# Performance work log

Measured on AMD Instinct MI355X. Metric: run time of the kernel, lower is better.

The kernel has to match this reference:

```python
import jax, jax.numpy as jnp
import numpy as np

UNITS = 100000
S = 64.0
M1 = 1.0
M2 = 0.5
M3 = 0.0


def setup_inputs() -> dict:
    key = jax.random.key(0)
    k1, k2, k3 = jax.random.split(key, 3)
    inputs = jax.random.normal(k1, (512, 512), dtype=jnp.float32)
    label = jax.random.randint(k2, (512,), 0, UNITS, dtype=jnp.int64)
    # fc7 weight, init stddev 0.01 as in the original layer
    w = jax.random.normal(k3, (512, UNITS), dtype=jnp.float32) * 0.01
    return {"inputs": inputs, "label": label, "w": w}


def reference(inputs, label, w):
    # L2-normalize embeddings (rows) and weights (columns)
    emb = inputs / jnp.linalg.norm(inputs, axis=-1, keepdims=True)
    wn = w / jnp.linalg.norm(w, axis=0, keepdims=True)
    # fc7 = s * cos(theta), shape [batch, units]
    fc7 = jnp.matmul(emb * S, wn)
    # ArcFace margin branch (m1=1.0, m2=0.5, m3=0.0)
    cos_t = fc7 / S
    t = jnp.arccos(cos_t)
    if M1 != 1.0:
        t = t * M1
    if M2 > 0.0:
        t = t + M2
    body = jnp.cos(t)
    if M3 > 0.0:
        body = body - M3
    diff = body * S - fc7
    one_hot = jax.nn.one_hot(label, UNITS, dtype=fc7.dtype)
    fc7 = fc7 + one_hot * diff
    return jax.nn.softmax(fc7, axis=-1)
```

## Files before the change

### kernel.cpp

```cpp
#include <hip/hip_runtime.h>
#include <math.h>

#define UNITS 100000
#define BATCH 512
#define DIM 512
#define BN 64
#define NBLK ((UNITS + BN - 1) / BN)
#define SCALE 64.0f
#define COS_M2 0.87758256189037271612f
#define SIN_M2 0.47942553860420300027f
#define LOG2E  1.44269504088896340736f

typedef _Float16 half8 __attribute__((ext_vector_type(8)));
typedef float floatx4 __attribute__((ext_vector_type(4)));

__global__ void norm_emb_k(const float* __restrict__ inp, _Float16* __restrict__ A2) {
    const int row = blockIdx.x;
    const int lane = threadIdx.x;
    const float* rp = inp + row * DIM + lane * 8;
    float v[8];
#pragma unroll
    for (int j = 0; j < 8; ++j) v[j] = rp[j];
    float ss = 0.f;
#pragma unroll
    for (int j = 0; j < 8; ++j) ss += v[j] * v[j];
#pragma unroll
    for (int off = 32; off > 0; off >>= 1) ss += __shfl_xor(ss, off);
    const float inv = 1.0f / sqrtf(ss);
    half8 h;
#pragma unroll
    for (int j = 0; j < 8; ++j) h[j] = (_Float16)(v[j] * inv);
    const int idx = ((((row >> 4) * 16 + (lane >> 2)) * 64) + (row & 15) + 16 * (lane & 3)) * 8;
    *(half8*)(A2 + idx) = h;
}

template<bool HALF>
__global__ __launch_bounds__(512, 4) void gemm_exp_k(
    const float* __restrict__ w, const _Float16* __restrict__ A2,
    const int* __restrict__ label,
    float* __restrict__ outf, _Float16* __restrict__ outh,
    float* __restrict__ psum, float* __restrict__ pmax) {
    __shared__ _Float16 Bt[64][64][8];
    __shared__ float scratch[32][68];
    __shared__ float cninv_s[64];

    const int t = threadIdx.x;
    const int blk = blockIdx.x;
    const int c0 = blk * BN;
    const int kk = t >> 4;
    const int ci = t & 15;

    bool valid[4];
#pragma unroll
    for (int j = 0; j < 4; ++j) valid[j] = (c0 + ci + 16 * j) < UNITS;

    float sq[4] = {0.f, 0.f, 0.f, 0.f};
    float va[4][4], vb[4][4];

    auto issue = [&](int g, float (*dst)[4]) {
#pragma unroll
        for (int c = 0; c < 4; ++c) {
            const float* p = w + (size_t)((g * 4 + c) * 32 + kk) * UNITS + c0 + ci;
#pragma unroll
            for (int j = 0; j < 4; ++j) dst[c][j] = valid[j] ? p[16 * j] : 0.f;
        }
    };
    auto consume = [&](int g, float (*src)[4]) {
#pragma unroll
        for (int c = 0; c < 4; ++c) {
            const int k = (g * 4 + c) * 32 + kk;
#pragma unroll
            for (int j = 0; j < 4; ++j) {
                const float x = src[c][j];
                sq[j] += x * x;
                Bt[k >> 3][ci + 16 * j][k & 7] = (_Float16)x;
            }
        }
    };
    issue(0, va);
    issue(1, vb);
    consume(0, va);
    issue(2, va);
    consume(1, vb);
    issue(3, vb);
    consume(2, va);
    consume(3, vb);

#pragma unroll
    for (int j = 0; j < 4; ++j) scratch[kk][ci + 16 * j] = sq[j];
    __syncthreads();
    if (t < 64) {
        float s = 0.f;
#pragma unroll
        for (int k2 = 0; k2 < 32; ++k2) s += scratch[k2][t];
        cninv_s[t] = 1.0f / sqrtf(s);
    }
    __syncthreads();

    const int wid = t >> 6;
    const int lane = t & 63;
    const int colg = lane & 15;
    const int rowg = lane >> 4;
    const int rowbase = wid * 64;

    floatx4 acc[4][4];
#pragma unroll
    for (int mf = 0; mf < 4; ++mf)
#pragma unroll
        for (int nf = 0; nf < 4; ++nf) acc[mf][nf] = (floatx4){0.f, 0.f, 0.f, 0.f};

#pragma unroll 2
    for (int ks = 0; ks < 16; ++ks) {
        half8 b[4];
#pragma unroll
        for (int nf = 0; nf < 4; ++nf)
            b[nf] = *(const half8*)(&Bt[ks * 4 + rowg][nf * 16 + colg][0]);
#pragma unroll
        for (int mf = 0; mf < 4; ++mf) {
            const half8 a = *(const half8*)(A2 + ((((wid * 4 + mf) * 16) + ks) * 64 + lane) * 8);
#pragma unroll
            for (int nf = 0; nf < 4; ++nf)
                acc[mf][nf] = __builtin_amdgcn_mfma_f32_16x16x32_f16(a, b[nf], acc[mf][nf], 0, 0, 0);
        }
    }

    float inv_cn[4];
#pragma unroll
    for (int nf = 0; nf < 4; ++nf) inv_cn[nf] = cninv_s[nf * 16 + colg];

#pragma unroll
    for (int mf = 0; mf < 4; ++mf) {
#pragma unroll
        for (int r = 0; r < 4; ++r) {
            const int R = rowbase + mf * 16 + rowg * 4 + r;
            const int labv = label[R];
            float lg[4];
            float mx = -1e30f;
#pragma unroll
            for (int nf = 0; nf < 4; ++nf) {
                const int C = c0 + nf * 16 + colg;
                float cs = acc[mf][nf][r] * inv_cn[nf];
                float x;
                if (C == labv) {
                    cs = fminf(1.f, fmaxf(-1.f, cs));
                    x = SCALE * (cs * COS_M2 - sqrtf(fmaxf(0.f, 1.f - cs * cs)) * SIN_M2);
                } else {
                    x = SCALE * cs;
                }
                if (C >= UNITS) x = -1e30f;
                lg[nf] = x;
                mx = fmaxf(mx, x);
            }
            mx = fmaxf(mx, __shfl_xor(mx, 1));
            mx = fmaxf(mx, __shfl_xor(mx, 2));
            mx = fmaxf(mx, __shfl_xor(mx, 4));
            mx = fmaxf(mx, __shfl_xor(mx, 8));
            float s = 0.f;
#pragma unroll
            for (int nf = 0; nf < 4; ++nf) {
                const int C = c0 + nf * 16 + colg;
                const float e = exp2f((lg[nf] - mx) * LOG2E);
                s += (C < UNITS) ? e : 0.f;
                if (C < UNITS) {
                    if (HALF) outh[(size_t)R * UNITS + C] = (_Float16)e;
                    else      outf[(size_t)R * UNITS + C] = e;
                }
            }
            s += __shfl_xor(s, 1);
            s += __shfl_xor(s, 2);
            s += __shfl_xor(s, 4);
            s += __shfl_xor(s, 8);
            if (colg == 0) {
                psum[R * NBLK + blk] = s;
                pmax[R * NBLK + blk] = mx;
            }
        }
    }
}

__global__ void rowfac_k(const float* __restrict__ psum, const float* __restrict__ pmax,
                         float* __restrict__ fac) {
    const int row = blockIdx.x;
    const int lane = threadIdx.x;
    float mx = -1e30f;
    for (int b = lane; b < NBLK; b += 64) mx = fmaxf(mx, pmax[row * NBLK + b]);
#pragma unroll
    for (int off = 32; off > 0; off >>= 1) mx = fmaxf(mx, __shfl_xor(mx, off));
    float s = 0.f;
    for (int b = lane; b < NBLK; b += 64)
        s += psum[row * NBLK + b] * exp2f((pmax[row * NBLK + b] - mx) * LOG2E);
#pragma unroll
    for (int off = 32; off > 0; off >>= 1) s += __shfl_xor(s, off);
    const float invS = 1.0f / s;
    for (int b = lane; b < NBLK; b += 64)
        fac[row * NBLK + b] = exp2f((pmax[row * NBLK + b] - mx) * LOG2E) * invS;
}

__global__ void scale_half_k(const _Float16* __restrict__ v, const float* __restrict__ fac,
                             float* __restrict__ out) {
    const int row = blockIdx.y;
    const int c = (blockIdx.x * 256 + threadIdx.x) * 8;
    if (c >= UNITS) return;
    const float f = fac[row * NBLK + (c >> 6)];
    const half8 h = *(const half8*)(v + (size_t)row * UNITS + c);
    float4 o1, o2;
    o1.x = (float)h[0] * f; o1.y = (float)h[1] * f; o1.z = (float)h[2] * f; o1.w = (float)h[3] * f;
    o2.x = (float)h[4] * f; o2.y = (float)h[5] * f; o2.z = (float)h[6] * f; o2.w = (float)h[7] * f;
    float* op = out + (size_t)row * UNITS + c;
    *(float4*)op = o1;
    *(float4*)(op + 4) = o2;
}

__global__ void scale_f32_k(float* __restrict__ out, const float* __restrict__ fac) {
    const int row = blockIdx.y;
    const int c = (blockIdx.x * 256 + threadIdx.x) * 8;
    if (c >= UNITS) return;
    const float f = fac[row * NBLK + (c >> 6)];
    float* op = out + (size_t)row * UNITS + c;
    float4 o1 = *(float4*)op;
    float4 o2 = *(float4*)(op + 4);
    o1.x *= f; o1.y *= f; o1.z *= f; o1.w *= f;
    o2.x *= f; o2.y *= f; o2.z *= f; o2.w *= f;
    *(float4*)op = o1;
    *(float4*)(op + 4) = o2;
}

extern "C" void kernel_launch(void* const* d_in, const int* in_sizes, int n_in,
                              void* d_out, int out_size, void* d_ws, size_t ws_size,
                              hipStream_t stream) {
    const float* inp   = (const float*)d_in[0];
    const int*   label = (const int*)d_in[1];
    const float* w     = (const float*)d_in[2];
    float* out = (float*)d_out;

    char* ws = (char*)d_ws;
    _Float16* A2   = (_Float16*)ws;
    float* psum    = (float*)(ws + (1 << 20));
    float* pmax    = (float*)(ws + (1 << 20) + 4 * BATCH * NBLK);
    float* fac     = (float*)(ws + (1 << 20) + 8 * BATCH * NBLK);
    _Float16* vh   = (_Float16*)(ws + (16 << 20));
    const size_t need = (size_t)(16 << 20) + (size_t)BATCH * UNITS * 2;
    const bool half_path = ws_size >= need;

    norm_emb_k<<<BATCH, 64, 0, stream>>>(inp, A2);
    if (half_path)
        gemm_exp_k<true><<<NBLK, 512, 0, stream>>>(w, A2, label, out, vh, psum, pmax);
    else
        gemm_exp_k<false><<<NBLK, 512, 0, stream>>>(w, A2, label, out, vh, psum, pmax);
    rowfac_k<<<BATCH, 64, 0, stream>>>(psum, pmax, fac);
    dim3 sg((UNITS + 2047) / 2048, BATCH);
    if (half_path)
        scale_half_k<<<sg, 256, 0, stream>>>(vh, fac, out);
    else
        scale_f32_k<<<sg, 256, 0, stream>>>(out, fac);
}
```

Before: 233.6 us.

## Pre-convert weights to fp16 tiles and stage GEMM outputs through LDS

Adds a separate wprep kernel that reads the fp32 weight matrix once. It computes the column inverse norms and writes an fp16 copy in the MFMA-ready tile layout. The GEMM kernel then loads each 64 KB tile straight into LDS with global_load_lds. Exponentials are written to a per-wave LDS bounce buffer first, so global stores become 16-byte vectors instead of scattered 2-byte writes, and the logit scale is folded into the embedding normalization. In exchange there is an extra kernel and an extra fp16 write and read of the whole weight matrix through HBM.

```diff
diff --git a/kernel.cpp b/kernel.cpp
--- a/kernel.cpp
+++ b/kernel.cpp
@@ -26,7 +26,7 @@
     for (int j = 0; j < 8; ++j) ss += v[j] * v[j];
 #pragma unroll
     for (int off = 32; off > 0; off >>= 1) ss += __shfl_xor(ss, off);
-    const float inv = 1.0f / sqrtf(ss);
+    const float inv = SCALE / sqrtf(ss);
     half8 h;
 #pragma unroll
     for (int j = 0; j < 8; ++j) h[j] = (_Float16)(v[j] * inv);
@@ -34,118 +34,129 @@
     *(half8*)(A2 + idx) = h;
 }
 
-template<bool HALF>
-__global__ __launch_bounds__(512, 4) void gemm_exp_k(
-    const float* __restrict__ w, const _Float16* __restrict__ A2,
-    const int* __restrict__ label,
-    float* __restrict__ outf, _Float16* __restrict__ outh,
-    float* __restrict__ psum, float* __restrict__ pmax) {
-    __shared__ _Float16 Bt[64][64][8];
-    __shared__ float scratch[32][68];
-    __shared__ float cninv_s[64];
-
+__global__ __launch_bounds__(256) void wprep_k(const float* __restrict__ w,
+                                               _Float16* __restrict__ w16,
+                                               float* __restrict__ cninv) {
+    __shared__ float T[128 * 66];
     const int t = threadIdx.x;
     const int blk = blockIdx.x;
     const int c0 = blk * BN;
-    const int kk = t >> 4;
-    const int ci = t & 15;
-
-    bool valid[4];
-#pragma unroll
-    for (int j = 0; j < 4; ++j) valid[j] = (c0 + ci + 16 * j) < UNITS;
-
-    float sq[4] = {0.f, 0.f, 0.f, 0.f};
-    float va[4][4], vb[4][4];
-
-    auto issue = [&](int g, float (*dst)[4]) {
-#pragma unroll
-        for (int c = 0; c < 4; ++c) {
-            const float* p = w + (size_t)((g * 4 + c) * 32 + kk) * UNITS + c0 + ci;
-#pragma unroll
-            for (int j = 0; j < 4; ++j) dst[c][j] = valid[j] ? p[16 * j] : 0.f;
-        }
-    };
-    auto consume = [&](int g, float (*src)[4]) {
-#pragma unroll
-        for (int c = 0; c < 4; ++c) {
-            const int k = (g * 4 + c) * 32 + kk;
-#pragma unroll
-            for (int j = 0; j < 4; ++j) {
-                const float x = src[c][j];
-                sq[j] += x * x;
-                Bt[k >> 3][ci + 16 * j][k & 7] = (_Float16)x;
-            }
-        }
-    };
-    issue(0, va);
-    issue(1, vb);
-    consume(0, va);
-    issue(2, va);
-    consume(1, vb);
-    issue(3, vb);
-    consume(2, va);
-    consume(3, vb);
-
-#pragma unroll
-    for (int j = 0; j < 4; ++j) scratch[kk][ci + 16 * j] = sq[j];
+    const int cl = (t & 31) * 2;
+    const int kr = t >> 5;
+    const bool cval = (c0 + cl + 1) < UNITS;
+    float sq0 = 0.f, sq1 = 0.f;
+
+    for (int q = 0; q < 4; ++q) {
+#pragma unroll
+        for (int ps = 0; ps < 16; ++ps) {
+            const int k = q * 128 + ps * 8 + kr;
+            float2 rd = cval ? *(const float2*)(w + (size_t)k * UNITS + c0 + cl)
+                             : make_float2(0.f, 0.f);
+            sq0 += rd.x * rd.x;
+            sq1 += rd.y * rd.y;
+            *(float2*)&T[(ps * 8 + kr) * 66 + cl] = rd;
+        }
+        __syncthreads();
+#pragma unroll
+        for (int g = 0; g < 4; ++g) {
+            const int G = t + 256 * g;
+            const int col = G & 63;
+            const int rowg = (G >> 6) & 3;
+            const int ksl = G >> 8;
+            half8 h;
+#pragma unroll
+            for (int e = 0; e < 8; ++e)
+                h[e] = (_Float16)T[(ksl * 32 + rowg * 8 + e) * 66 + col];
+            const int off = blk * 32768 + (((q * 4 + ksl) * 4 + rowg) * 64 + col) * 8;
+            *(half8*)(w16 + off) = h;
+        }
+        __syncthreads();
+    }
+    T[(t >> 5) * 66 + cl] = sq0;
+    T[(t >> 5) * 66 + cl + 1] = sq1;
     __syncthreads();
     if (t < 64) {
         float s = 0.f;
 #pragma unroll
-        for (int k2 = 0; k2 < 32; ++k2) s += scratch[k2][t];
-        cninv_s[t] = 1.0f / sqrtf(s);
-    }
-    __syncthreads();
-
+        for (int gi = 0; gi < 8; ++gi) s += T[gi * 66 + t];
+        cninv[c0 + t] = (s > 0.f) ? rsqrtf(s) : 1.0f;
+    }
+}
+
+template<bool HALF>
+__global__ __launch_bounds__(512, 4) void gemm2_k(
+    const _Float16* __restrict__ w16, const _Float16* __restrict__ A2,
+    const int* __restrict__ label, const float* __restrict__ cninv,
+    float* __restrict__ outf, _Float16* __restrict__ vh,
+    float* __restrict__ psum, float* __restrict__ pmax) {
+    __shared__ char smem[73728];
+    _Float16* Bt = (_Float16*)smem;
+
+    const int t = threadIdx.x;
+    const int blk = blockIdx.x;
+    const int c0 = blk * BN;
     const int wid = t >> 6;
     const int lane = t & 63;
     const int colg = lane & 15;
     const int rowg = lane >> 4;
     const int rowbase = wid * 64;
 
+    const char* gsrc = (const char*)w16 + (size_t)blk * 65536;
+#pragma unroll
+    for (int j = 0; j < 8; ++j) {
+        const int chunk = wid * 8 + j;
+        __builtin_amdgcn_global_load_lds(
+            (const __attribute__((address_space(1))) void*)(gsrc + chunk * 1024 + lane * 16),
+            (__attribute__((address_space(3))) void*)(smem + chunk * 1024 + lane * 16),
+            16, 0, 0);
+    }
+
+    float cn[4];
+#pragma unroll
+    for (int nf = 0; nf < 4; ++nf) cn[nf] = cninv[c0 + nf * 16 + colg];
+
+    asm volatile("s_waitcnt vmcnt(0)" ::: "memory");
+    __syncthreads();
+
     floatx4 acc[4][4];
 #pragma unroll
     for (int mf = 0; mf < 4; ++mf)
 #pragma unroll
         for (int nf = 0; nf < 4; ++nf) acc[mf][nf] = (floatx4){0.f, 0.f, 0.f, 0.f};
 
-#pragma unroll 2
+#pragma unroll 4
     for (int ks = 0; ks < 16; ++ks) {
         half8 b[4];
 #pragma unroll
         for (int nf = 0; nf < 4; ++nf)
-            b[nf] = *(const half8*)(&Bt[ks * 4 + rowg][nf * 16 + colg][0]);
+            b[nf] = *(const half8*)(Bt + ((ks * 4 + rowg) * 64 + nf * 16 + colg) * 8);
 #pragma unroll
         for (int mf = 0; mf < 4; ++mf) {
-            const half8 a = *(const half8*)(A2 + ((((wid * 4 + mf) * 16) + ks) * 64 + lane) * 8);
+            const half8 a = *(const half8*)(A2 + (((wid * 4 + mf) * 16 + ks) * 64 + lane) * 8);
 #pragma unroll
             for (int nf = 0; nf < 4; ++nf)
                 acc[mf][nf] = __builtin_amdgcn_mfma_f32_16x16x32_f16(a, b[nf], acc[mf][nf], 0, 0, 0);
         }
     }
-
-    float inv_cn[4];
-#pragma unroll
-    for (int nf = 0; nf < 4; ++nf) inv_cn[nf] = cninv_s[nf * 16 + colg];
-
+    __syncthreads();
+
+    _Float16* bounce = (_Float16*)smem + wid * 4608;
 #pragma unroll
     for (int mf = 0; mf < 4; ++mf) {
 #pragma unroll
         for (int r = 0; r < 4; ++r) {
-            const int R = rowbase + mf * 16 + rowg * 4 + r;
+            const int lrow = mf * 16 + rowg * 4 + r;
+            const int R = rowbase + lrow;
             const int labv = label[R];
             float lg[4];
             float mx = -1e30f;
 #pragma unroll
             for (int nf = 0; nf < 4; ++nf) {
                 const int C = c0 + nf * 16 + colg;
-                float cs = acc[mf][nf][r] * inv_cn[nf];
-                float x;
+                float x = acc[mf][nf][r] * cn[nf];
                 if (C == labv) {
-                    cs = fminf(1.f, fmaxf(-1.f, cs));
+                    float cs = fminf(1.f, fmaxf(-1.f, x * (1.0f / SCALE)));
                     x = SCALE * (cs * COS_M2 - sqrtf(fmaxf(0.f, 1.f - cs * cs)) * SIN_M2);
-                } else {
-                    x = SCALE * cs;
                 }
                 if (C >= UNITS) x = -1e30f;
                 lg[nf] = x;
@@ -161,10 +172,7 @@
                 const int C = c0 + nf * 16 + colg;
                 const float e = exp2f((lg[nf] - mx) * LOG2E);
                 s += (C < UNITS) ? e : 0.f;
-                if (C < UNITS) {
-                    if (HALF) outh[(size_t)R * UNITS + C] = (_Float16)e;
-                    else      outf[(size_t)R * UNITS + C] = e;
-                }
+                bounce[lrow * 72 + nf * 16 + colg] = (_Float16)e;
             }
             s += __shfl_xor(s, 1);
             s += __shfl_xor(s, 2);
@@ -173,6 +181,29 @@
             if (colg == 0) {
                 psum[R * NBLK + blk] = s;
                 pmax[R * NBLK + blk] = mx;
+            }
+        }
+    }
+    __syncthreads();
+
+    const int rl = lane >> 3;
+    const int ch = lane & 7;
+#pragma unroll
+    for (int p = 0; p < 8; ++p) {
+        const int row_l = p * 8 + rl;
+        const int Rg = rowbase + row_l;
+        const int C8 = c0 + ch * 8;
+        const half8 h = *(const half8*)((_Float16*)smem + wid * 4608 + row_l * 72 + ch * 8);
+        if (C8 + 7 < UNITS) {
+            if (HALF) {
+                *(half8*)(vh + (size_t)Rg * UNITS + C8) = h;
+            } else {
+                float4 o1, o2;
+                o1.x = (float)h[0]; o1.y = (float)h[1]; o1.z = (float)h[2]; o1.w = (float)h[3];
+                o2.x = (float)h[4]; o2.y = (float)h[5]; o2.z = (float)h[6]; o2.w = (float)h[7];
+                float* op = outf + (size_t)Rg * UNITS + C8;
+                *(float4*)op = o1;
+                *(float4*)(op + 4) = o2;
             }
         }
     }
@@ -236,17 +267,20 @@
     char* ws = (char*)d_ws;
     _Float16* A2   = (_Float16*)ws;
     float* psum    = (float*)(ws + (1 << 20));
-    float* pmax    = (float*)(ws + (1 << 20) + 4 * BATCH * NBLK);
-    float* fac     = (float*)(ws + (1 << 20) + 8 * BATCH * NBLK);
-    _Float16* vh   = (_Float16*)(ws + (16 << 20));
-    const size_t need = (size_t)(16 << 20) + (size_t)BATCH * UNITS * 2;
+    float* pmax    = (float*)(ws + (1 << 20) + 4u * BATCH * NBLK);
+    float* fac     = (float*)(ws + (1 << 20) + 8u * BATCH * NBLK);
+    float* cninv   = (float*)(ws + (1 << 20) + 12u * BATCH * NBLK);
+    _Float16* w16  = (_Float16*)(ws + (16 << 20));
+    _Float16* vh   = (_Float16*)(ws + (size_t)(16 << 20) + (size_t)NBLK * 65536);
+    const size_t need = (size_t)(16 << 20) + (size_t)NBLK * 65536 + (size_t)BATCH * UNITS * 2;
     const bool half_path = ws_size >= need;
 
     norm_emb_k<<<BATCH, 64, 0, stream>>>(inp, A2);
+    wprep_k<<<NBLK, 256, 0, stream>>>(w, w16, cninv);
     if (half_path)
-        gemm_exp_k<true><<<NBLK, 512, 0, stream>>>(w, A2, label, out, vh, psum, pmax);
+        gemm2_k<true><<<NBLK, 512, 0, stream>>>(w16, A2, label, cninv, out, vh, psum, pmax);
     else
-        gemm_exp_k<false><<<NBLK, 512, 0, stream>>>(w, A2, label, out, vh, psum, pmax);
+        gemm2_k<false><<<NBLK, 512, 0, stream>>>(w16, A2, label, cninv, out, vh, psum, pmax);
     rowfac_k<<<BATCH, 64, 0, stream>>>(psum, pmax, fac);
     dim3 sg((UNITS + 2047) / 2048, BATCH);
     if (half_path)
```

Result: slower. 325.9 us (+39.5%).

## Pipeline weight loads with MFMA via double-buffered LDS and coalesce half stores

Applied to the files above, without the earlier changes.

The GEMM kernel now streams the weight columns in eight K-chunks through a double-buffered LDS tile, so global loads for later chunks overlap with MFMA work on the current chunk. Before, all loads and conversions finished before any matrix math started. The fp16 exp values are staged through LDS and written out as 16-byte row segments instead of scattered 2-byte stores. The per-block partial sums and maxima are written transposed and contiguous, and the scale factor is folded into embedding normalisation. The cost is more barriers and extra LDS traffic, plus a 16-byte store path that assumes the unit count is a multiple of 8.

```diff
diff --git a/kernel.cpp b/kernel.cpp
--- a/kernel.cpp
+++ b/kernel.cpp
@@ -14,6 +14,11 @@
 typedef _Float16 half8 __attribute__((ext_vector_type(8)));
 typedef float floatx4 __attribute__((ext_vector_type(4)));
 
+#define PHASE_BARRIER() do { \
+    asm volatile("s_waitcnt lgkmcnt(0)" ::: "memory"); \
+    __builtin_amdgcn_s_barrier(); \
+} while (0)
+
 __global__ void norm_emb_k(const float* __restrict__ inp, _Float16* __restrict__ A2) {
     const int row = blockIdx.x;
     const int lane = threadIdx.x;
@@ -26,7 +31,7 @@
     for (int j = 0; j < 8; ++j) ss += v[j] * v[j];
 #pragma unroll
     for (int off = 32; off > 0; off >>= 1) ss += __shfl_xor(ss, off);
-    const float inv = 1.0f / sqrtf(ss);
+    const float inv = SCALE / sqrtf(ss);
     half8 h;
 #pragma unroll
     for (int j = 0; j < 8; ++j) h[j] = (_Float16)(v[j] * inv);
@@ -35,117 +40,114 @@
 }
 
 template<bool HALF>
-__global__ __launch_bounds__(512, 4) void gemm_exp_k(
+__global__ __launch_bounds__(512, 4) void gemmfused_k(
     const float* __restrict__ w, const _Float16* __restrict__ A2,
     const int* __restrict__ label,
-    float* __restrict__ outf, _Float16* __restrict__ outh,
+    _Float16* __restrict__ vh, float* __restrict__ outf,
     float* __restrict__ psum, float* __restrict__ pmax) {
-    __shared__ _Float16 Bt[64][64][8];
-    __shared__ float scratch[32][68];
+    __shared__ _Float16 Bt[2][512 * 8];
+    __shared__ float sqred[8][64];
     __shared__ float cninv_s[64];
+    __shared__ float sums_s[512];
+    __shared__ float maxs_s[512];
 
     const int t = threadIdx.x;
     const int blk = blockIdx.x;
     const int c0 = blk * BN;
-    const int kk = t >> 4;
-    const int ci = t & 15;
-
-    bool valid[4];
-#pragma unroll
-    for (int j = 0; j < 4; ++j) valid[j] = (c0 + ci + 16 * j) < UNITS;
-
-    float sq[4] = {0.f, 0.f, 0.f, 0.f};
-    float va[4][4], vb[4][4];
-
-    auto issue = [&](int g, float (*dst)[4]) {
-#pragma unroll
-        for (int c = 0; c < 4; ++c) {
-            const float* p = w + (size_t)((g * 4 + c) * 32 + kk) * UNITS + c0 + ci;
-#pragma unroll
-            for (int j = 0; j < 4; ++j) dst[c][j] = valid[j] ? p[16 * j] : 0.f;
-        }
+    const int w8 = t >> 6;
+    const int lane = t & 63;
+    const int colg = lane & 15;
+    const int rowg = lane >> 4;
+
+    const bool cval = (c0 + lane) < UNITS;
+    const float* wbase = w + (cval ? (c0 + lane) : (UNITS - 1));
+
+    float sq = 0.f;
+    float rs[2][8];
+
+    auto LOADC = [&](int ch, float* r) {
+#pragma unroll
+        for (int i = 0; i < 8; ++i)
+            r[i] = wbase[(size_t)(ch * 64 + w8 * 8 + i) * UNITS];
     };
-    auto consume = [&](int g, float (*src)[4]) {
-#pragma unroll
-        for (int c = 0; c < 4; ++c) {
-            const int k = (g * 4 + c) * 32 + kk;
-#pragma unroll
-            for (int j = 0; j < 4; ++j) {
-                const float x = src[c][j];
-                sq[j] += x * x;
-                Bt[k >> 3][ci + 16 * j][k & 7] = (_Float16)x;
-            }
-        }
+    auto WRITEC = [&](const float* r, int buf) {
+        half8 h;
+#pragma unroll
+        for (int i = 0; i < 8; ++i) {
+            const float x = cval ? r[i] : 0.f;
+            sq += x * x;
+            h[i] = (_Float16)x;
+        }
+        *(half8*)&Bt[buf][(w8 * 64 + lane) * 8] = h;
     };
-    issue(0, va);
-    issue(1, vb);
-    consume(0, va);
-    issue(2, va);
-    consume(1, vb);
-    issue(3, vb);
-    consume(2, va);
-    consume(3, vb);
-
-#pragma unroll
-    for (int j = 0; j < 4; ++j) scratch[kk][ci + 16 * j] = sq[j];
+
+    floatx4 acc[4][4];
+#pragma unroll
+    for (int mf = 0; mf < 4; ++mf)
+#pragma unroll
+        for (int nf = 0; nf < 4; ++nf) acc[mf][nf] = (floatx4){0.f, 0.f, 0.f, 0.f};
+
+    auto MFMAC = [&](int ch, int buf) {
+#pragma unroll
+        for (int ksl = 0; ksl < 2; ++ksl) {
+            half8 b[4];
+#pragma unroll
+            for (int nf = 0; nf < 4; ++nf)
+                b[nf] = *(const half8*)&Bt[buf][((ksl * 4 + rowg) * 64 + nf * 16 + colg) * 8];
+#pragma unroll
+            for (int mf = 0; mf < 4; ++mf) {
+                const half8 a = *(const half8*)(A2 +
+                    (size_t)(((w8 * 4 + mf) * 16 + ch * 2 + ksl) * 64 + lane) * 8);
+#pragma unroll
+                for (int nf = 0; nf < 4; ++nf)
+                    acc[mf][nf] = __builtin_amdgcn_mfma_f32_16x16x32_f16(a, b[nf], acc[mf][nf], 0, 0, 0);
+            }
+        }
+    };
+
+    LOADC(0, rs[0]);
+    LOADC(1, rs[1]);
+    WRITEC(rs[0], 0);
+    PHASE_BARRIER();
+#pragma unroll
+    for (int ch = 0; ch < 8; ++ch) {
+        if (ch + 2 < 8) LOADC(ch + 2, rs[ch & 1]);
+        if (ch + 1 < 8) WRITEC(rs[1 - (ch & 1)], (ch + 1) & 1);
+        MFMAC(ch, ch & 1);
+        PHASE_BARRIER();
+    }
+
+    sqred[w8][lane] = sq;
     __syncthreads();
     if (t < 64) {
         float s = 0.f;
 #pragma unroll
-        for (int k2 = 0; k2 < 32; ++k2) s += scratch[k2][t];
-        cninv_s[t] = 1.0f / sqrtf(s);
+        for (int g = 0; g < 8; ++g) s += sqred[g][t];
+        cninv_s[t] = rsqrtf(s);
     }
     __syncthreads();
 
-    const int wid = t >> 6;
-    const int lane = t & 63;
-    const int colg = lane & 15;
-    const int rowg = lane >> 4;
-    const int rowbase = wid * 64;
-
-    floatx4 acc[4][4];
-#pragma unroll
-    for (int mf = 0; mf < 4; ++mf)
-#pragma unroll
-        for (int nf = 0; nf < 4; ++nf) acc[mf][nf] = (floatx4){0.f, 0.f, 0.f, 0.f};
-
-#pragma unroll 2
-    for (int ks = 0; ks < 16; ++ks) {
-        half8 b[4];
-#pragma unroll
-        for (int nf = 0; nf < 4; ++nf)
-            b[nf] = *(const half8*)(&Bt[ks * 4 + rowg][nf * 16 + colg][0]);
-#pragma unroll
-        for (int mf = 0; mf < 4; ++mf) {
-            const half8 a = *(const half8*)(A2 + ((((wid * 4 + mf) * 16) + ks) * 64 + lane) * 8);
-#pragma unroll
-            for (int nf = 0; nf < 4; ++nf)
-                acc[mf][nf] = __builtin_amdgcn_mfma_f32_16x16x32_f16(a, b[nf], acc[mf][nf], 0, 0, 0);
-        }
-    }
-
-    float inv_cn[4];
-#pragma unroll
-    for (int nf = 0; nf < 4; ++nf) inv_cn[nf] = cninv_s[nf * 16 + colg];
+    float cn[4];
+#pragma unroll
+    for (int nf = 0; nf < 4; ++nf) cn[nf] = cninv_s[nf * 16 + colg];
+
+    _Float16* bounce = &Bt[0][0] + w8 * 1024;
 
 #pragma unroll
     for (int mf = 0; mf < 4; ++mf) {
 #pragma unroll
         for (int r = 0; r < 4; ++r) {
-            const int R = rowbase + mf * 16 + rowg * 4 + r;
+            const int R = w8 * 64 + mf * 16 + rowg * 4 + r;
             const int labv = label[R];
             float lg[4];
             float mx = -1e30f;
 #pragma unroll
             for (int nf = 0; nf < 4; ++nf) {
                 const int C = c0 + nf * 16 + colg;
-                float cs = acc[mf][nf][r] * inv_cn[nf];
-                float x;
+                float x = acc[mf][nf][r] * cn[nf];
                 if (C == labv) {
-                    cs = fminf(1.f, fmaxf(-1.f, cs));
+                    float cs = fminf(1.f, fmaxf(-1.f, x * (1.0f / SCALE)));
                     x = SCALE * (cs * COS_M2 - sqrtf(fmaxf(0.f, 1.f - cs * cs)) * SIN_M2);
-                } else {
-                    x = SCALE * cs;
                 }
                 if (C >= UNITS) x = -1e30f;
                 lg[nf] = x;
@@ -161,21 +163,31 @@
                 const int C = c0 + nf * 16 + colg;
                 const float e = exp2f((lg[nf] - mx) * LOG2E);
                 s += (C < UNITS) ? e : 0.f;
-                if (C < UNITS) {
-                    if (HALF) outh[(size_t)R * UNITS + C] = (_Float16)e;
-                    else      outf[(size_t)R * UNITS + C] = e;
-                }
+                if (HALF) bounce[(rowg * 4 + r) * 64 + nf * 16 + colg] = (_Float16)e;
+                else if (C < UNITS) outf[(size_t)R * UNITS + C] = e;
             }
             s += __shfl_xor(s, 1);
             s += __shfl_xor(s, 2);
             s += __shfl_xor(s, 4);
             s += __shfl_xor(s, 8);
-            if (colg == 0) {
-                psum[R * NBLK + blk] = s;
-                pmax[R * NBLK + blk] = mx;
+            if (colg == 0) { sums_s[R] = s; maxs_s[R] = mx; }
+        }
+        if (HALF) {
+#pragma unroll
+            for (int p = 0; p < 2; ++p) {
+                const int row_l = p * 8 + (lane >> 3);
+                const int seg = lane & 7;
+                const half8 hv = *(const half8*)&bounce[row_l * 64 + seg * 8];
+                const int gc = c0 + seg * 8;
+                if (gc + 8 <= UNITS)
+                    *(half8*)(vh + (size_t)(w8 * 64 + mf * 16 + row_l) * UNITS + gc) = hv;
             }
         }
     }
+
+    __syncthreads();
+    psum[(size_t)blk * BATCH + t] = sums_s[t];
+    pmax[(size_t)blk * BATCH + t] = maxs_s[t];
 }
 
 __global__ void rowfac_k(const float* __restrict__ psum, const float* __restrict__ pmax,
@@ -183,17 +195,17 @@
     const int row = blockIdx.x;
     const int lane = threadIdx.x;
     float mx = -1e30f;
-    for (int b = lane; b < NBLK; b += 64) mx = fmaxf(mx, pmax[row * NBLK + b]);
+    for (int b = lane; b < NBLK; b += 64) mx = fmaxf(mx, pmax[(size_t)b * BATCH + row]);
 #pragma unroll
     for (int off = 32; off > 0; off >>= 1) mx = fmaxf(mx, __shfl_xor(mx, off));
     float s = 0.f;
     for (int b = lane; b < NBLK; b += 64)
-        s += psum[row * NBLK + b] * exp2f((pmax[row * NBLK + b] - mx) * LOG2E);
+        s += psum[(size_t)b * BATCH + row] * exp2f((pmax[(size_t)b * BATCH + row] - mx) * LOG2E);
 #pragma unroll
     for (int off = 32; off > 0; off >>= 1) s += __shfl_xor(s, off);
     const float invS = 1.0f / s;
     for (int b = lane; b < NBLK; b += 64)
-        fac[row * NBLK + b] = exp2f((pmax[row * NBLK + b] - mx) * LOG2E) * invS;
+        fac[(size_t)row * NBLK + b] = exp2f((pmax[(size_t)b * BATCH + row] - mx) * LOG2E) * invS;
 }
 
 __global__ void scale_half_k(const _Float16* __restrict__ v, const float* __restrict__ fac,
@@ -201,7 +213,7 @@
     const int row = blockIdx.y;
     const int c = (blockIdx.x * 256 + threadIdx.x) * 8;
     if (c >= UNITS) return;
-    const float f = fac[row * NBLK + (c >> 6)];
+    const float f = fac[(size_t)row * NBLK + (c >> 6)];
     const half8 h = *(const half8*)(v + (size_t)row * UNITS + c);
     float4 o1, o2;
     o1.x = (float)h[0] * f; o1.y = (float)h[1] * f; o1.z = (float)h[2] * f; o1.w = (float)h[3] * f;
@@ -215,7 +227,7 @@
     const int row = blockIdx.y;
     const int c = (blockIdx.x * 256 + threadIdx.x) * 8;
     if (c >= UNITS) return;
-    const float f = fac[row * NBLK + (c >> 6)];
+    const float f = fac[(size_t)row * NBLK + (c >> 6)];
     float* op = out + (size_t)row * UNITS + c;
     float4 o1 = *(float4*)op;
     float4 o2 = *(float4*)(op + 4);
@@ -234,19 +246,19 @@
     float* out = (float*)d_out;
 
     char* ws = (char*)d_ws;
-    _Float16* A2   = (_Float16*)ws;
-    float* psum    = (float*)(ws + (1 << 20));
-    float* pmax    = (float*)(ws + (1 << 20) + 4 * BATCH * NBLK);
-    float* fac     = (float*)(ws + (1 << 20) + 8 * BATCH * NBLK);
-    _Float16* vh   = (_Float16*)(ws + (16 << 20));
-    const size_t need = (size_t)(16 << 20) + (size_t)BATCH * UNITS * 2;
+    _Float16* A2 = (_Float16*)ws;
+    float* psum  = (float*)(ws + (4u << 20));
+    float* pmax  = (float*)(ws + (8u << 20));
+    float* fac   = (float*)(ws + (12u << 20));
+    _Float16* vh = (_Float16*)(ws + (16u << 20));
+    const size_t need = (size_t)(16u << 20) + (size_t)BATCH * UNITS * 2;
     const bool half_path = ws_size >= need;
 
     norm_emb_k<<<BATCH, 64, 0, stream>>>(inp, A2);
     if (half_path)
-        gemm_exp_k<true><<<NBLK, 512, 0, stream>>>(w, A2, label, out, vh, psum, pmax);
+        gemmfused_k<true><<<NBLK, 512, 0, stream>>>(w, A2, label, vh, out, psum, pmax);
     else
-        gemm_exp_k<false><<<NBLK, 512, 0, stream>>>(w, A2, label, out, vh, psum, pmax);
+        gemmfused_k<false><<<NBLK, 512, 0, stream>>>(w, A2, label, vh, out, psum, pmax);
     rowfac_k<<<BATCH, 64, 0, stream>>>(psum, pmax, fac);
     dim3 sg((UNITS + 2047) / 2048, BATCH);
     if (half_path)
```

Measured after the change: 267.2 us. 1.14x slower.

## Stage half-precision exp tiles through LDS and coalesce stores with padded stride

Applied to the files above, without the earlier changes.

Each wave now writes its exp values into an LDS bounce buffer and stores them as 16-byte nontemporal rows into a half buffer padded to a 16-byte-aligned row stride. Per-block sums and maxes are gathered in shared memory and written transposed so stores are coalesced. A-fragments are prefetched one k-step ahead, the column-norm reduction overlaps the first A load, and the scale factor S is folded into the embedding normalization. Scale kernels use nontemporal loads and stores. The cost is extra LDS traffic and barriers, and rowfac now reads strided partials.

```diff
diff --git a/kernel.cpp b/kernel.cpp
--- a/kernel.cpp
+++ b/kernel.cpp
@@ -6,6 +6,7 @@
 #define DIM 512
 #define BN 64
 #define NBLK ((UNITS + BN - 1) / BN)
+#define VSTRIDE 100096
 #define SCALE 64.0f
 #define COS_M2 0.87758256189037271612f
 #define SIN_M2 0.47942553860420300027f
@@ -26,7 +27,7 @@
     for (int j = 0; j < 8; ++j) ss += v[j] * v[j];
 #pragma unroll
     for (int off = 32; off > 0; off >>= 1) ss += __shfl_xor(ss, off);
-    const float inv = 1.0f / sqrtf(ss);
+    const float inv = SCALE / sqrtf(ss);
     half8 h;
 #pragma unroll
     for (int j = 0; j < 8; ++j) h[j] = (_Float16)(v[j] * inv);
@@ -38,11 +39,13 @@
 __global__ __launch_bounds__(512, 4) void gemm_exp_k(
     const float* __restrict__ w, const _Float16* __restrict__ A2,
     const int* __restrict__ label,
-    float* __restrict__ outf, _Float16* __restrict__ outh,
+    float* __restrict__ outf, _Float16* __restrict__ vh,
     float* __restrict__ psum, float* __restrict__ pmax) {
     __shared__ _Float16 Bt[64][64][8];
     __shared__ float scratch[32][68];
     __shared__ float cninv_s[64];
+    __shared__ float sums_s[512];
+    __shared__ float maxs_s[512];
 
     const int t = threadIdx.x;
     const int blk = blockIdx.x;
@@ -88,14 +91,6 @@
 
 #pragma unroll
     for (int j = 0; j < 4; ++j) scratch[kk][ci + 16 * j] = sq[j];
-    __syncthreads();
-    if (t < 64) {
-        float s = 0.f;
-#pragma unroll
-        for (int k2 = 0; k2 < 32; ++k2) s += scratch[k2][t];
-        cninv_s[t] = 1.0f / sqrtf(s);
-    }
-    __syncthreads();
 
     const int wid = t >> 6;
     const int lane = t & 63;
@@ -103,6 +98,19 @@
     const int rowg = lane >> 4;
     const int rowbase = wid * 64;
 
+    half8 ap[4];
+#pragma unroll
+    for (int mf = 0; mf < 4; ++mf)
+        ap[mf] = *(const half8*)(A2 + ((((wid * 4 + mf) * 16) + 0) * 64 + lane) * 8);
+
+    __syncthreads();
+    if (t < 64) {
+        float s = 0.f;
+#pragma unroll
+        for (int k2 = 0; k2 < 32; ++k2) s += scratch[k2][t];
+        cninv_s[t] = 1.0f / sqrtf(s);
+    }
+
     floatx4 acc[4][4];
 #pragma unroll
     for (int mf = 0; mf < 4; ++mf)
@@ -115,37 +123,44 @@
 #pragma unroll
         for (int nf = 0; nf < 4; ++nf)
             b[nf] = *(const half8*)(&Bt[ks * 4 + rowg][nf * 16 + colg][0]);
-#pragma unroll
-        for (int mf = 0; mf < 4; ++mf) {
-            const half8 a = *(const half8*)(A2 + ((((wid * 4 + mf) * 16) + ks) * 64 + lane) * 8);
+        half8 a[4];
+#pragma unroll
+        for (int mf = 0; mf < 4; ++mf) a[mf] = ap[mf];
+        if (ks < 15) {
+#pragma unroll
+            for (int mf = 0; mf < 4; ++mf)
+                ap[mf] = *(const half8*)(A2 + ((((wid * 4 + mf) * 16) + ks + 1) * 64 + lane) * 8);
+        }
+#pragma unroll
+        for (int mf = 0; mf < 4; ++mf)
 #pragma unroll
             for (int nf = 0; nf < 4; ++nf)
-                acc[mf][nf] = __builtin_amdgcn_mfma_f32_16x16x32_f16(a, b[nf], acc[mf][nf], 0, 0, 0);
-        }
+                acc[mf][nf] = __builtin_amdgcn_mfma_f32_16x16x32_f16(a[mf], b[nf], acc[mf][nf], 0, 0, 0);
     }
-
-    float inv_cn[4];
-#pragma unroll
-    for (int nf = 0; nf < 4; ++nf) inv_cn[nf] = cninv_s[nf * 16 + colg];
+    __syncthreads();
+
+    float cn[4];
+#pragma unroll
+    for (int nf = 0; nf < 4; ++nf) cn[nf] = cninv_s[nf * 16 + colg];
+
+    _Float16* bounce = &Bt[0][0][0] + wid * 1152;
 
 #pragma unroll
     for (int mf = 0; mf < 4; ++mf) {
 #pragma unroll
         for (int r = 0; r < 4; ++r) {
-            const int R = rowbase + mf * 16 + rowg * 4 + r;
+            const int lrow = mf * 16 + rowg * 4 + r;
+            const int R = rowbase + lrow;
             const int labv = label[R];
             float lg[4];
             float mx = -1e30f;
 #pragma unroll
             for (int nf = 0; nf < 4; ++nf) {
                 const int C = c0 + nf * 16 + colg;
-                float cs = acc[mf][nf][r] * inv_cn[nf];
-                float x;
+                float x = acc[mf][nf][r] * cn[nf];
                 if (C == labv) {
-                    cs = fminf(1.f, fmaxf(-1.f, cs));
+                    float cs = fminf(1.f, fmaxf(-1.f, x * (1.0f / SCALE)));
                     x = SCALE * (cs * COS_M2 - sqrtf(fmaxf(0.f, 1.f - cs * cs)) * SIN_M2);
-                } else {
-                    x = SCALE * cs;
                 }
                 if (C >= UNITS) x = -1e30f;
                 lg[nf] = x;
@@ -161,21 +176,32 @@
                 const int C = c0 + nf * 16 + colg;
                 const float e = exp2f((lg[nf] - mx) * LOG2E);
                 s += (C < UNITS) ? e : 0.f;
-                if (C < UNITS) {
-                    if (HALF) outh[(size_t)R * UNITS + C] = (_Float16)e;
-                    else      outf[(size_t)R * UNITS + C] = e;
-                }
+                if (HALF) bounce[(rowg * 4 + r) * 72 + nf * 16 + colg] = (_Float16)e;
+                else if (C < UNITS) outf[(size_t)R * UNITS + C] = e;
             }
             s += __shfl_xor(s, 1);
             s += __shfl_xor(s, 2);
             s += __shfl_xor(s, 4);
             s += __shfl_xor(s, 8);
-            if (colg == 0) {
-                psum[R * NBLK + blk] = s;
-                pmax[R * NBLK + blk] = mx;
+            if (colg == 0) { sums_s[R] = s; maxs_s[R] = mx; }
+        }
+        if (HALF) {
+#pragma unroll
+            for (int p = 0; p < 2; ++p) {
+                const int row_l = p * 8 + (lane >> 3);
+                const int seg = lane & 7;
+                const int gc = c0 + seg * 8;
+                const half8 hv = *(const half8*)&bounce[row_l * 72 + seg * 8];
+                if (gc + 8 <= UNITS)
+                    __builtin_nontemporal_store(hv,
+                        (half8*)(vh + (size_t)(rowbase + mf * 16 + row_l) * VSTRIDE + gc));
             }
         }
     }
+
+    __syncthreads();
+    __builtin_nontemporal_store(sums_s[t], &psum[(size_t)blk * BATCH + t]);
+    __builtin_nontemporal_store(maxs_s[t], &pmax[(size_t)blk * BATCH + t]);
 }
 
 __global__ void rowfac_k(const float* __restrict__ psum, const float* __restrict__ pmax,
@@ -183,17 +209,18 @@
     const int row = blockIdx.x;
     const int lane = threadIdx.x;
     float mx = -1e30f;
-    for (int b = lane; b < NBLK; b += 64) mx = fmaxf(mx, pmax[row * NBLK + b]);
+    for (int b = lane; b < NBLK; b += 64)
+        mx = fmaxf(mx, pmax[(size_t)b * BATCH + row]);
 #pragma unroll
     for (int off = 32; off > 0; off >>= 1) mx = fmaxf(mx, __shfl_xor(mx, off));
     float s = 0.f;
     for (int b = lane; b < NBLK; b += 64)
-        s += psum[row * NBLK + b] * exp2f((pmax[row * NBLK + b] - mx) * LOG2E);
+        s += psum[(size_t)b * BATCH + row] * exp2f((pmax[(size_t)b * BATCH + row] - mx) * LOG2E);
 #pragma unroll
     for (int off = 32; off > 0; off >>= 1) s += __shfl_xor(s, off);
     const float invS = 1.0f / s;
     for (int b = lane; b < NBLK; b += 64)
-        fac[row * NBLK + b] = exp2f((pmax[row * NBLK + b] - mx) * LOG2E) * invS;
+        fac[(size_t)row * NBLK + b] = exp2f((pmax[(size_t)b * BATCH + row] - mx) * LOG2E) * invS;
 }
 
 __global__ void scale_half_k(const _Float16* __restrict__ v, const float* __restrict__ fac,
@@ -201,28 +228,28 @@
     const int row = blockIdx.y;
     const int c = (blockIdx.x * 256 + threadIdx.x) * 8;
     if (c >= UNITS) return;
-    const float f = fac[row * NBLK + (c >> 6)];
-    const half8 h = *(const half8*)(v + (size_t)row * UNITS + c);
-    float4 o1, o2;
-    o1.x = (float)h[0] * f; o1.y = (float)h[1] * f; o1.z = (float)h[2] * f; o1.w = (float)h[3] * f;
-    o2.x = (float)h[4] * f; o2.y = (float)h[5] * f; o2.z = (float)h[6] * f; o2.w = (float)h[7] * f;
+    const float f = fac[(size_t)row * NBLK + (c >> 6)];
+    const half8 h = __builtin_nontemporal_load((const half8*)(v + (size_t)row * VSTRIDE + c));
+    floatx4 o1, o2;
+#pragma unroll
+    for (int j = 0; j < 4; ++j) { o1[j] = (float)h[j] * f; o2[j] = (float)h[4 + j] * f; }
     float* op = out + (size_t)row * UNITS + c;
-    *(float4*)op = o1;
-    *(float4*)(op + 4) = o2;
+    __builtin_nontemporal_store(o1, (floatx4*)op);
+    __builtin_nontemporal_store(o2, (floatx4*)(op + 4));
 }
 
 __global__ void scale_f32_k(float* __restrict__ out, const float* __restrict__ fac) {
     const int row = blockIdx.y;
     const int c = (blockIdx.x * 256 + threadIdx.x) * 8;
     if (c >= UNITS) return;
-    const float f = fac[row * NBLK + (c >> 6)];
+    const float f = fac[(size_t)row * NBLK + (c >> 6)];
     float* op = out + (size_t)row * UNITS + c;
-    float4 o1 = *(float4*)op;
-    float4 o2 = *(float4*)(op + 4);
-    o1.x *= f; o1.y *= f; o1.z *= f; o1.w *= f;
-    o2.x *= f; o2.y *= f; o2.z *= f; o2.w *= f;
-    *(float4*)op = o1;
-    *(float4*)(op + 4) = o2;
+    floatx4 o1 = *(floatx4*)op;
+    floatx4 o2 = *(floatx4*)(op + 4);
+#pragma unroll
+    for (int j = 0; j < 4; ++j) { o1[j] *= f; o2[j] *= f; }
+    *(floatx4*)op = o1;
+    *(floatx4*)(op + 4) = o2;
 }
 
 extern "C" void kernel_launch(void* const* d_in, const int* in_sizes, int n_in,
@@ -234,12 +261,12 @@
     float* out = (float*)d_out;
 
     char* ws = (char*)d_ws;
-    _Float16* A2   = (_Float16*)ws;
-    float* psum    = (float*)(ws + (1 << 20));
-    float* pmax    = (float*)(ws + (1 << 20) + 4 * BATCH * NBLK);
-    float* fac     = (float*)(ws + (1 << 20) + 8 * BATCH * NBLK);
-    _Float16* vh   = (_Float16*)(ws + (16 << 20));
-    const size_t need = (size_t)(16 << 20) + (size_t)BATCH * UNITS * 2;
+    _Float16* A2 = (_Float16*)ws;
+    float* psum  = (float*)(ws + (4u << 20));
+    float* pmax  = (float*)(ws + (8u << 20));
+    float* fac   = (float*)(ws + (12u << 20));
+    _Float16* vh = (_Float16*)(ws + (16u << 20));
+    const size_t need = (size_t)(16u << 20) + (size_t)BATCH * VSTRIDE * 2;
     const bool half_path = ws_size >= need;
 
     norm_emb_k<<<BATCH, 64, 0, stream>>>(inp, A2);
@@ -248,7 +275,7 @@
     else
         gemm_exp_k<false><<<NBLK, 512, 0, stream>>>(w, A2, label, out, vh, psum, pmax);
     rowfac_k<<<BATCH, 64, 0, stream>>>(psum, pmax, fac);
-    dim3 sg((UNITS + 2047) / 2048, BATCH);
+    dim3 sg((UNITS / 8 + 255) / 256, BATCH);
     if (half_path)
         scale_half_k<<<sg, 256, 0, stream>>>(vh, fac, out);
     else
```

After: 250.8 us. +7.4%, slower.
